# Performance work log

Hardware: AMD Instinct MI355X
Metric: run time of the kernel (lower is better)

Reference implementation:

```python
import jax, jax.numpy as jnp
from jax import lax
import numpy as np

ATTN = 32  # attn_size window
PAD, SOS = 1, 2


def setup_inputs() -> dict:
    key = jax.random.key(0)
    ks = jax.random.split(key, 20)
    B, L, V, E, H = 16, 64, 32000, 512, 512
    sc = 0.02
    inp = {
        "s_tensor": jax.random.randint(ks[0], (B, L), 0, V, dtype=jnp.int32),
        "parents_tensor": jax.random.randint(ks[1], (L,), 0, L, dtype=jnp.int32),
        "emb": jax.random.normal(ks[2], (V, E), jnp.float32) * sc,
        "W_hid": jax.random.normal(ks[3], (H, H), jnp.float32) * sc,
        "b_hid": jnp.zeros((H,), jnp.float32),
        "v_w": jax.random.normal(ks[4], (H,), jnp.float32) * sc,
        "v_b": jnp.zeros((1,), jnp.float32),
        "W_ctx": jax.random.normal(ks[5], (E + H, H), jnp.float32) * sc,
        "b_ctx": jnp.zeros((H,), jnp.float32),
        "W_ih": jax.random.normal(ks[6], (H, 4 * H), jnp.float32) * sc,
        "W_hh": jax.random.normal(ks[7], (H, 4 * H), jnp.float32) * sc,
        "b_lstm": jnp.zeros((4 * H,), jnp.float32),
        "W_glob": jax.random.normal(ks[8], (3 * H, V), jnp.float32) * sc,
        "b_glob": jnp.zeros((V,), jnp.float32),
        "w_sw": jax.random.normal(ks[9], (2 * H,), jnp.float32) * sc,
        "b_sw": jnp.zeros((1,), jnp.float32),
    }
    return inp


def _decode(emb, W_hid, b_hid, v_w, v_b, W_ctx, b_ctx, W_ih, W_hh, b_lstm,
            W_glob, b_glob, w_sw, b_sw, s_tensor, parents_tensor):
    B, L = s_tensor.shape
    H = W_hid.shape[0]
    A = ATTN
    # teacher forcing: input at step t is SOS for t=0, else s_tensor[:, t-1]
    inputs = jnp.concatenate(
        [jnp.full((B, 1), SOS, s_tensor.dtype), s_tensor[:, : L - 2]], axis=1)  # [B, L-1]
    targets = s_tensor[:, 1:]  # [B, L-1]
    hs_buf0 = jnp.zeros((B, A + L, H), jnp.float32)  # past decoder hidden states (A zero-pad prefix)
    h0 = jnp.zeros((B, H), jnp.float32)
    c0 = jnp.zeros((B, H), jnp.float32)

    def step(carry, xs):
        h, c, hs_buf = carry
        tok, tgt, par, t = xs
        x = emb[tok]  # [B, E]
        # memory = last A decoder hidden states (steps t-A .. t-1)
        mem = lax.dynamic_slice(hs_buf, (0, t, 0), (B, A, H))
        # Bahdanau-style scores: v^T tanh(W_hidden(h) + mem), masked to valid window
        q = h @ W_hid + b_hid  # [B, H]
        scores = jnp.tanh(q[:, None, :] + mem) @ v_w + v_b  # [B, A]
        valid = jnp.arange(A) >= (A - t)
        scores = jnp.where(valid[None, :], scores, -1e20)
        attn = jax.nn.softmax(scores, axis=1)
        context = jnp.einsum('ba,bah->bh', attn, mem)
        hid = jax.nn.selu(jnp.concatenate([x, context], axis=1) @ W_ctx + b_ctx)
        # single-step LSTM cell (PyTorch gate order i,f,g,o)
        gates = hid @ W_ih + h @ W_hh + b_lstm
        i, f, g, o = jnp.split(gates, 4, axis=1)
        c_new = jax.nn.sigmoid(f) * c + jax.nn.sigmoid(i) * jnp.tanh(g)
        h_new = jax.nn.sigmoid(o) * jnp.tanh(c_new)
        # parent hidden state
        p = jnp.clip(par, 0, jnp.maximum(t - 1, 0))
        h_par = lax.dynamic_slice(hs_buf, (0, A + p, 0), (B, 1, H))[:, 0]
        logits = jnp.concatenate([h_new, c_new, h_par], axis=1) @ W_glob + b_glob
        logp = jax.nn.log_softmax(logits, axis=1)
        s = jax.nn.sigmoid(jnp.concatenate([h_new, c_new], axis=1) @ w_sw + b_sw)  # [B,1]
        out = s[:, None] * logp if s.ndim == 1 else s * logp  # pointer switch on global dist
        nll = -jnp.take_along_axis(out, tgt[:, None].astype(jnp.int32), axis=1)[:, 0]
        nll = jnp.where(tgt != PAD, nll, 0.0)
        pred = jnp.argmax(out, axis=1).astype(jnp.int32)
        hs_buf = lax.dynamic_update_slice(hs_buf, h_new[:, None, :], (0, A + t, 0))
        return (h_new, c_new, hs_buf), (nll, pred)

    T = L - 1
    xs = (inputs.T, targets.T, parents_tensor[:T], jnp.arange(T, dtype=jnp.int32))
    _, (nlls, preds) = lax.scan(step, (h0, c0, hs_buf0), xs)
    loss = nlls.sum() / B
    return loss, preds.T  # [B, L-1] predicted tokens


def reference(s_tensor, parents_tensor, emb, W_hid, b_hid, v_w, v_b, W_ctx, b_ctx,
              W_ih, W_hh, b_lstm, W_glob, b_glob, w_sw, b_sw):
    return _decode(emb, W_hid, b_hid, v_w, v_b, W_ctx, b_ctx, W_ih, W_hh, b_lstm,
                   W_glob, b_glob, w_sw, b_sw, s_tensor, parents_tensor)
```

## Files before the change

kernel.cpp:

```cpp
#include <hip/hip_runtime.h>
#include <math.h>

#define BB 16
#define LL 64
#define TT 63
#define HH 512
#define AA 32
#define VV 32000
#define NCHUNK 250
#define CHW 128
#define TGRP 3
#define PAD_TOK 1
#define SOS_TOK 2
#define HSROW 96
#define ZK 1536
#define FLTMAX 3.402823466e38f

__device__ __forceinline__ float sigm(float x){ return 1.0f/(1.0f + __expf(-x)); }

__global__ __launch_bounds__(256) void k_pre(const int* __restrict__ s, const float* __restrict__ emb,
                      const float* __restrict__ Wctx, const float* __restrict__ bctx,
                      float* __restrict__ xwpre)
{
    int t = blockIdx.x >> 3;
    int jc = blockIdx.x & 7;
    int tid = threadIdx.x;
    int jj = tid & 63, bq = tid >> 6;
    int j = jc*64 + jj;
    __shared__ int toks[BB];
    __shared__ float xs[BB][HH];
    if (tid < BB) {
        int b = tid;
        toks[b] = (t == 0) ? SOS_TOK : s[b*LL + (t-1)];
    }
    __syncthreads();
    for (int i = tid; i < BB*HH; i += 256) {
        int b = i >> 9, k = i & 511;
        xs[b][k] = emb[(size_t)toks[b]*HH + k];
    }
    __syncthreads();
    float acc[4];
    #pragma unroll
    for (int u = 0; u < 4; u++) acc[u] = bctx[j];
    for (int k = 0; k < HH; k += 4) {
        float w0 = Wctx[(k+0)*HH+j], w1 = Wctx[(k+1)*HH+j],
              w2 = Wctx[(k+2)*HH+j], w3 = Wctx[(k+3)*HH+j];
        #pragma unroll
        for (int u = 0; u < 4; u++) {
            int b = bq*4 + u;
            float4 hv = *reinterpret_cast<const float4*>(&xs[b][k]);
            acc[u] = fmaf(hv.x, w0, acc[u]);
            acc[u] = fmaf(hv.y, w1, acc[u]);
            acc[u] = fmaf(hv.z, w2, acc[u]);
            acc[u] = fmaf(hv.w, w3, acc[u]);
        }
    }
    #pragma unroll
    for (int u = 0; u < 4; u++) {
        int b = bq*4 + u;
        xwpre[((size_t)t*BB + b)*HH + j] = acc[u];
    }
}

__global__ __launch_bounds__(256) void k_tw(const float* __restrict__ Wg, float4* __restrict__ Wt4b)
{
    int kg = blockIdx.x / 125;
    int cb = blockIdx.x % 125;
    int col = cb*256 + threadIdx.x;
    const float* w0 = Wg + (size_t)(4*kg)*VV + col;
    float4 v;
    v.x = w0[0];
    v.y = w0[VV];
    v.z = w0[2*VV];
    v.w = w0[3*VV];
    Wt4b[(size_t)(col >> 6)*(384*64) + kg*64 + (col & 63)] = v;
}

__global__ __launch_bounds__(256) void k_twl(const float* __restrict__ W, float4* __restrict__ WT)
{
    int kg = blockIdx.x >> 3;
    int cb = blockIdx.x & 7;
    int col = cb*256 + threadIdx.x;
    const float* w0 = W + (size_t)(4*kg)*2048 + col;
    float4 v;
    v.x = w0[0];
    v.y = w0[2048];
    v.z = w0[2*2048];
    v.w = w0[3*2048];
    WT[(size_t)kg*2048 + col] = v;
}

__device__ void finish_step(int tp, int b, int tid,
                            const int* __restrict__ s,
                            const float* __restrict__ lb,
                            const float* __restrict__ pmax,
                            const float* __restrict__ spart,
                            const float* __restrict__ bsw,
                            float* __restrict__ nll, float* __restrict__ out,
                            float* cv, int* ci, double* sdd, float* extra)
{
    float v = -FLTMAX;
    if (tid < NCHUNK) v = pmax[tid*BB + b];
    cv[tid] = v; __syncthreads();
    for (int sft = 256; sft >= 1; sft >>= 1) {
        if (tid < sft) cv[tid] = fmaxf(cv[tid], cv[tid+sft]);
        __syncthreads();
    }
    float gmax = cv[0];
    __syncthreads();

    const float* Lb = lb + (size_t)b*VV;
    double sd = 0.0;
    for (int col = tid; col < VV; col += 512) {
        float d1 = Lb[col] - gmax;
        double u = (double)d1, e;
        if (u < -0.25) {
            e = exp(u);
        } else {
            e = 1.0 + u*(1.0/7.0);
            e = 1.0 + u*e*(1.0/6.0);
            e = 1.0 + u*e*(1.0/5.0);
            e = 1.0 + u*e*(1.0/4.0);
            e = 1.0 + u*e*(1.0/3.0);
            e = 1.0 + u*e*(1.0/2.0);
            e = 1.0 + u*e;
        }
        sd += e;
    }
    sdd[tid] = sd; __syncthreads();
    for (int sft = 256; sft >= 1; sft >>= 1) {
        if (tid < sft) sdd[tid] += sdd[tid+sft];
        __syncthreads();
    }
    float logS = logf((float)sdd[0]);

    float z = bsw[0];
    #pragma unroll
    for (int i2 = 0; i2 < 8; i2++) z += spart[b*8 + i2];
    float sF = 1.0f/(1.0f + expf(-z));
    __syncthreads();

    int tg = s[b*LL + tp + 1];
    float best = -FLTMAX; int bidx = 0x7fffffff;
    for (int col = tid; col < VV; col += 512) {
        float d1 = Lb[col] - gmax;
        float d2 = d1 - logS;
        float pq = sF * d2;
        if (pq > best) { best = pq; bidx = col; }
        if (col == tg) extra[0] = pq;
    }
    cv[tid] = best; ci[tid] = bidx; __syncthreads();
    for (int sft = 256; sft >= 1; sft >>= 1) {
        if (tid < sft) {
            float v2 = cv[tid+sft]; int i2 = ci[tid+sft];
            if (v2 > cv[tid] || (v2 == cv[tid] && i2 < ci[tid])) { cv[tid] = v2; ci[tid] = i2; }
        }
        __syncthreads();
    }
    if (tid == 0) {
        out[1 + b*TT + tp] = (float)ci[0];
        nll[tp*BB + b] = (tg != PAD_TOK) ? -extra[0] : 0.f;
    }
    __syncthreads();
}

__global__ __launch_bounds__(512) void k_fin_all(
    int t0, const int* __restrict__ s,
    const float* __restrict__ lbBase, unsigned long long lbStride,
    const float* __restrict__ pmaxBase, unsigned long long pmaxStride,
    const float* __restrict__ spartAll, const float* __restrict__ bsw,
    float* __restrict__ nll, float* __restrict__ out)
{
    __shared__ float cv[512];
    __shared__ int   ci[512];
    __shared__ double sdd[512];
    __shared__ float extra[2];
    int idx = blockIdx.x >> 4;
    int tp = t0 + idx, b = blockIdx.x & 15;
    finish_step(tp, b, threadIdx.x, s,
                lbBase + (size_t)idx * lbStride,
                pmaxBase + (size_t)idx * pmaxStride,
                spartAll + (size_t)tp * 128,
                bsw, nll, out, cv, ci, sdd, extra);
}

__global__ __launch_bounds__(512) void k_attn(
    int t,
    const float* __restrict__ Whid, const float* __restrict__ bhid,
    const float* __restrict__ vw, const float* __restrict__ vb,
    const float* __restrict__ Wctx, const float* __restrict__ xwpre,
    const float* __restrict__ hs, float* __restrict__ hidg)
{
    int b = blockIdx.x, tid = threadIdx.x;
    __shared__ float hsh[HH], qs[HH], ctxs[HH];
    __shared__ float sc[AA], at[AA];
    const float* hp = hs + ((size_t)b*HSROW + (AA + t - 1))*HH;
    hsh[tid] = hp[tid];
    __syncthreads();
    {
        int j = tid;
        float acc = bhid[j];
        for (int k = 0; k < HH; k += 4) {
            float4 hv = *reinterpret_cast<const float4*>(&hsh[k]);
            acc = fmaf(hv.x, Whid[(k+0)*HH+j], acc);
            acc = fmaf(hv.y, Whid[(k+1)*HH+j], acc);
            acc = fmaf(hv.z, Whid[(k+2)*HH+j], acc);
            acc = fmaf(hv.w, Whid[(k+3)*HH+j], acc);
        }
        qs[j] = acc;
    }
    __syncthreads();
    {
        int w = tid >> 6, lane = tid & 63;
        for (int r = 0; r < 4; r++) {
            int a = w + 8*r;
            const float* mem = hs + ((size_t)b*HSROW + (t + a))*HH;
            float p = 0.f;
            for (int j = lane; j < HH; j += 64) p += tanhf(qs[j] + mem[j]) * vw[j];
            for (int m = 32; m >= 1; m >>= 1) p += __shfl_xor(p, m);
            if (lane == 0) sc[a] = (a >= AA - t) ? (p + vb[0]) : -1e20f;
        }
    }
    __syncthreads();
    if (tid < 64) {
        float v = (tid < 32) ? sc[tid] : -FLTMAX;
        float m = v;
        for (int sh = 16; sh >= 1; sh >>= 1) m = fmaxf(m, __shfl_xor(m, sh));
        float e = (tid < 32) ? __expf(v - m) : 0.f;
        float ss = e;
        for (int sh = 16; sh >= 1; sh >>= 1) ss += __shfl_xor(ss, sh);
        if (tid < 32) at[tid] = e / ss;
    }
    __syncthreads();
    {
        int j = tid;
        float ctx = 0.f;
        for (int a = 0; a < AA; a++)
            ctx += at[a] * hs[((size_t)b*HSROW + (t + a))*HH + j];
        ctxs[j] = ctx;
    }
    __syncthreads();
    {
        int j = tid;
        float acc = xwpre[((size_t)t*BB + b)*HH + j];
        const float* W2 = Wctx + (size_t)HH*HH;
        for (int k = 0; k < HH; k += 4) {
            float4 hv = *reinterpret_cast<const float4*>(&ctxs[k]);
            acc = fmaf(hv.x, W2[(k+0)*HH+j], acc);
            acc = fmaf(hv.y, W2[(k+1)*HH+j], acc);
            acc = fmaf(hv.z, W2[(k+2)*HH+j], acc);
            acc = fmaf(hv.w, W2[(k+3)*HH+j], acc);
        }
        const float scl = 1.0507009873554805f, al = 1.6732632423543772f;
        hidg[b*HH + j] = (acc > 0.f) ? scl*acc : scl*al*expm1f(acc);
    }
}

__global__ __launch_bounds__(256) void k_gates(
    int t, const int* __restrict__ parents,
    const float4* __restrict__ WihT, const float4* __restrict__ WhhT,
    const float* __restrict__ blstm, const float* __restrict__ wsw,
    const float* __restrict__ hidg, float* __restrict__ hs,
    float* __restrict__ cvec, float* __restrict__ spart,
    float* __restrict__ zbuf)
{
    int bid = blockIdx.x, b = bid >> 3, hc = bid & 7, h0 = hc*64;
    int tid = threadIdx.x, g = tid >> 6, jj = tid & 63, j = h0 + jj, col = g*HH + j;
    __shared__ float hid_s[HH], h_s[HH];
    __shared__ float gsl[4][64];
    const float* hp = hs + ((size_t)b*HSROW + (AA + t - 1))*HH;
    for (int k = tid; k < HH; k += 256) { hid_s[k] = hidg[b*HH + k]; h_s[k] = hp[k]; }
    __syncthreads();
    float acc = blstm[col];
    #pragma unroll 8
    for (int kg = 0; kg < 128; kg++) {
        float4 w = WihT[(size_t)kg*2048 + col];
        float4 hv = *reinterpret_cast<const float4*>(&hid_s[kg*4]);
        acc = fmaf(hv.x, w.x, acc);
        acc = fmaf(hv.y, w.y, acc);
        acc = fmaf(hv.z, w.z, acc);
        acc = fmaf(hv.w, w.w, acc);
    }
    #pragma unroll 8
    for (int kg = 0; kg < 128; kg++) {
        float4 w = WhhT[(size_t)kg*2048 + col];
        float4 hv = *reinterpret_cast<const float4*>(&h_s[kg*4]);
        acc = fmaf(hv.x, w.x, acc);
        acc = fmaf(hv.y, w.y, acc);
        acc = fmaf(hv.z, w.z, acc);
        acc = fmaf(hv.w, w.w, acc);
    }
    gsl[g][jj] = acc;
    __syncthreads();
    if (tid >= 64 && tid < 128) {
        int jj2 = tid - 64;
        int par = parents[t];
        int tm1 = (t - 1 > 0) ? (t - 1) : 0;
        int p = (par < 0) ? 0 : ((par > tm1) ? tm1 : par);
        float v = (t == 0) ? 0.f : hs[((size_t)b*HSROW + (AA + p))*HH + h0 + jj2];
        zbuf[(size_t)b*ZK + 2*HH + h0 + jj2] = v;
    }
    if (tid < 64) {
        float gi = gsl[0][jj], gf = gsl[1][jj], gg = gsl[2][jj], go = gsl[3][jj];
        float cp = cvec[b*HH + j];
        float cn = sigm(gf)*cp + sigm(gi)*tanhf(gg);
        float hn = sigm(go)*tanhf(cn);
        cvec[b*HH + j] = cn;
        hs[((size_t)b*HSROW + (AA + t))*HH + j] = hn;
        zbuf[(size_t)b*ZK + j] = hn;
        zbuf[(size_t)b*ZK + HH + j] = cn;
        float sp = hn*wsw[j] + cn*wsw[HH + j];
        for (int m = 32; m >= 1; m >>= 1) sp += __shfl_xor(sp, m);
        if (jj == 0) spart[b*8 + hc] = sp;
    }
}

template<int NT>
__device__ __forceinline__ void logits_body2(
    const float4* __restrict__ Wt4b, const float* __restrict__ bg,
    const float* __restrict__ zBase, size_t zStride,
    float* __restrict__ lbBase, size_t lbStride,
    float* __restrict__ pmaxBase, size_t pmaxStride)
{
    int tid = threadIdx.x;
    int chunk = blockIdx.y;
    int lane = tid & 63;
    int cg = lane & 31;
    int kh = lane >> 5;
    int b0 = (tid >> 6) * 4;
    int base_t = blockIdx.x * NT;

    const float4* wt0 = Wt4b + (size_t)(chunk*2 + 0)*(384*64) + cg;
    const float4* wt1 = Wt4b + (size_t)(chunk*2 + 0)*(384*64) + cg + 32;
    const float4* wt2 = Wt4b + (size_t)(chunk*2 + 1)*(384*64) + cg;
    const float4* wt3 = Wt4b + (size_t)(chunk*2 + 1)*(384*64) + cg + 32;

    float acc[NT][4][4];
    #pragma unroll
    for (int tt = 0; tt < NT; tt++)
        #pragma unroll
        for (int cc = 0; cc < 4; cc++) {
            float binit = (kh == 0) ? bg[chunk*CHW + cg + 32*cc] : 0.f;
            #pragma unroll
            for (int u = 0; u < 4; u++) acc[tt][cc][u] = binit;
        }

    for (int kc = 0; kc < 3; kc++) {
        const float* zb[NT];
        #pragma unroll
        for (int tt = 0; tt < NT; tt++)
            zb[tt] = zBase + (size_t)(base_t + tt)*zStride + kc*512 + (size_t)b0*ZK;
        int kgb = kc*128 + kh*64;
        #pragma unroll 2
        for (int k4 = 0; k4 < 64; k4++) {
            int kb = kh*256 + k4*4;
            size_t wof = (size_t)(kgb + k4)*64;
            float4 w0 = wt0[wof];
            float4 w1 = wt1[wof];
            float4 w2 = wt2[wof];
            float4 w3 = wt3[wof];
            #pragma unroll
            for (int tt = 0; tt < NT; tt++) {
                #pragma unroll
                for (int u = 0; u < 4; u++) {
                    float4 z = *reinterpret_cast<const float4*>(&zb[tt][(size_t)u*ZK + kb]);
                    acc[tt][0][u] = fmaf(z.x, w0.x, fmaf(z.y, w0.y, fmaf(z.z, w0.z, fmaf(z.w, w0.w, acc[tt][0][u]))));
                    acc[tt][1][u] = fmaf(z.x, w1.x, fmaf(z.y, w1.y, fmaf(z.z, w1.z, fmaf(z.w, w1.w, acc[tt][1][u]))));
                    acc[tt][2][u] = fmaf(z.x, w2.x, fmaf(z.y, w2.y, fmaf(z.z, w2.z, fmaf(z.w, w2.w, acc[tt][2][u]))));
                    acc[tt][3][u] = fmaf(z.x, w3.x, fmaf(z.y, w3.y, fmaf(z.z, w3.z, fmaf(z.w, w3.w, acc[tt][3][u]))));
                }
            }
        }
    }

    #pragma unroll
    for (int tt = 0; tt < NT; tt++) {
        float* lb   = lbBase   + (size_t)(base_t + tt)*lbStride;
        float* pmax = pmaxBase + (size_t)(base_t + tt)*pmaxStride;
        #pragma unroll
        for (int u = 0; u < 4; u++) {
            float vmax = -FLTMAX;
            #pragma unroll
            for (int cc = 0; cc < 4; cc++) {
                float a = acc[tt][cc][u];
                float oth = __shfl_xor(a, 32);
                float tot = a + oth;
                if (kh == 0) lb[(size_t)(b0 + u)*VV + chunk*CHW + cg + 32*cc] = tot;
                vmax = fmaxf(vmax, tot);
            }
            for (int m = 16; m >= 1; m >>= 1) vmax = fmaxf(vmax, __shfl_xor(vmax, m));
            if (lane == 0) pmax[chunk*BB + b0 + u] = vmax;
        }
    }
}

__global__ __launch_bounds__(256) void k_logits_mega3(
    const float4* __restrict__ Wt4b, const float* __restrict__ bg,
    const float* __restrict__ zBase,
    float* __restrict__ lbBase, float* __restrict__ pmaxBase)
{
    logits_body2<TGRP>(Wt4b, bg, zBase, (size_t)BB*ZK, lbBase, 512000, pmaxBase, 4000);
}

__global__ __launch_bounds__(256) void k_logits_T1(
    const float4* __restrict__ Wt4b, const float* __restrict__ bg,
    const float* __restrict__ zbuf,
    float* __restrict__ lb, float* __restrict__ pmax)
{
    logits_body2<1>(Wt4b, bg, zbuf, 0, lb, 0, pmax, 0);
}

__global__ __launch_bounds__(256) void k_logits_F(
    const float* __restrict__ Wg, const float* __restrict__ bg,
    const float* __restrict__ zbuf,
    float* __restrict__ lb, float* __restrict__ pmax)
{
    int tid = threadIdx.x;
    int chunk = blockIdx.y;
    int lane = tid & 63;
    int cg = lane & 31;
    int kh = lane >> 5;
    int b0 = (tid >> 6) * 4;

    float acc[4][4];
    #pragma unroll
    for (int cc = 0; cc < 4; cc++) {
        float binit = (kh == 0) ? bg[chunk*CHW + cg + 32*cc] : 0.f;
        #pragma unroll
        for (int u = 0; u < 4; u++) acc[cc][u] = binit;
    }

    for (int kc = 0; kc < 3; kc++) {
        const float* zb = zbuf + kc*512 + (size_t)b0*ZK;
        #pragma unroll 2
        for (int k4 = 0; k4 < 64; k4++) {
            int kb = kh*256 + k4*4;
            const float* wr = Wg + (size_t)(kc*512 + kb)*VV + chunk*CHW + cg;
            float4 w[4];
            #pragma unroll
            for (int cc = 0; cc < 4; cc++) {
                w[cc].x = wr[32*cc];
                w[cc].y = wr[(size_t)VV + 32*cc];
                w[cc].z = wr[(size_t)2*VV + 32*cc];
                w[cc].w = wr[(size_t)3*VV + 32*cc];
            }
            #pragma unroll
            for (int u = 0; u < 4; u++) {
                float4 z = *reinterpret_cast<const float4*>(&zb[(size_t)u*ZK + kb]);
                #pragma unroll
                for (int cc = 0; cc < 4; cc++)
                    acc[cc][u] = fmaf(z.x, w[cc].x, fmaf(z.y, w[cc].y, fmaf(z.z, w[cc].z, fmaf(z.w, w[cc].w, acc[cc][u]))));
            }
        }
    }

    #pragma unroll
    for (int u = 0; u < 4; u++) {
        float vmax = -FLTMAX;
        #pragma unroll
        for (int cc = 0; cc < 4; cc++) {
            float a = acc[cc][u];
            float oth = __shfl_xor(a, 32);
            float tot = a + oth;
            if (kh == 0) lb[(size_t)(b0 + u)*VV + chunk*CHW + cg + 32*cc] = tot;
            vmax = fmaxf(vmax, tot);
        }
        for (int m = 16; m >= 1; m >>= 1) vmax = fmaxf(vmax, __shfl_xor(vmax, m));
        if (lane == 0) pmax[chunk*BB + b0 + u] = vmax;
    }
}

__global__ __launch_bounds__(256) void k_final_loss(
    const float* __restrict__ nll, float* __restrict__ out)
{
    __shared__ double cs2[256];
    int tid = threadIdx.x;
    double psm = 0.0;
    for (int i = tid; i < TT*BB; i += 256) psm += (double)nll[i];
    cs2[tid] = psm; __syncthreads();
    for (int sft = 128; sft >= 1; sft >>= 1) {
        if (tid < sft) cs2[tid] += cs2[tid+sft];
        __syncthreads();
    }
    if (tid == 0) out[0] = (float)(cs2[0] / (double)BB);
}

extern "C" void kernel_launch(void* const* d_in, const int* in_sizes, int n_in,
                              void* d_out, int out_size, void* d_ws, size_t ws_size,
                              hipStream_t stream)
{
    const int*   s_tok = (const int*)  d_in[0];
    const int*   par   = (const int*)  d_in[1];
    const float* emb   = (const float*)d_in[2];
    const float* Whid  = (const float*)d_in[3];
    const float* bhid  = (const float*)d_in[4];
    const float* vw    = (const float*)d_in[5];
    const float* vb    = (const float*)d_in[6];
    const float* Wctx  = (const float*)d_in[7];
    const float* bctx  = (const float*)d_in[8];
    const float* Wih   = (const float*)d_in[9];
    const float* Whh   = (const float*)d_in[10];
    const float* blstm = (const float*)d_in[11];
    const float* Wg    = (const float*)d_in[12];
    const float* bg    = (const float*)d_in[13];
    const float* wsw   = (const float*)d_in[14];
    const float* bsw   = (const float*)d_in[15];
    float* out = (float*)d_out;

    size_t ws_f = ws_size / sizeof(float);
    const size_t base_f = 786432 + 8192 + 516096 + 8192;
    const size_t com_f  = 8064 + 1008 + 2*1048576;
    const size_t full_f = base_f + com_f + (size_t)63*4000 + (size_t)63*512000
                        + (size_t)63*24576 + 49152000;
    const size_t mid_f  = base_f + com_f + 4000 + 512000 + 24576 + 49152000;
    int mode = (ws_f >= full_f) ? 2 : ((ws_f >= mid_f) ? 1 : 0);

    float* ws = (float*)d_ws;
    size_t off = 0;
    float* hs      = ws + off; off += 786432;
    float* cvec    = ws + off; off += 8192;
    float* xwpre   = ws + off; off += 516096;
    float* hidg    = ws + off; off += 8192;
    float* pmaxAll = ws + off; off += (mode == 2) ? (size_t)63*4000 : 4000;
    float* spartAll= ws + off; off += 8064;
    float* nll     = ws + off; off += 1008;
    float* zbufAll = ws + off; off += (mode == 2) ? (size_t)63*24576 : 24576;
    float* lbAll   = ws + off; off += (mode == 2) ? (size_t)63*512000 : 512000;
    float4* WihT   = (float4*)(ws + off); off += 1048576;
    float4* WhhT   = (float4*)(ws + off); off += 1048576;
    float4* Wt4b   = (float4*)(ws + off);

    hipMemsetAsync(hs, 0, (786432 + 8192) * sizeof(float), stream);

    hipLaunchKernelGGL(k_twl, dim3(1024), dim3(256), 0, stream, Wih, WihT);
    hipLaunchKernelGGL(k_twl, dim3(1024), dim3(256), 0, stream, Whh, WhhT);
    if (mode >= 1) {
        hipLaunchKernelGGL(k_tw, dim3(384*125), dim3(256), 0, stream, Wg, Wt4b);
    }
    hipLaunchKernelGGL(k_pre, dim3(TT*8), dim3(256), 0, stream, s_tok, emb, Wctx, bctx, xwpre);

    if (mode == 2) {
        for (int t = 0; t < TT; t++) {
            hipLaunchKernelGGL(k_attn, dim3(BB), dim3(512), 0, stream,
                t, Whid, bhid, vw, vb, Wctx, xwpre, hs, hidg);
            hipLaunchKernelGGL(k_gates, dim3(128), dim3(256), 0, stream,
                t, par, WihT, WhhT, blstm, wsw, hidg, hs, cvec,
                spartAll + (size_t)t*128, zbufAll + (size_t)t*BB*ZK);
        }
        hipLaunchKernelGGL(k_logits_mega3, dim3(TT/TGRP, NCHUNK), dim3(256), 0, stream,
            Wt4b, bg, zbufAll, lbAll, pmaxAll);
        hipLaunchKernelGGL(k_fin_all, dim3(TT*BB), dim3(512), 0, stream,
            0, s_tok, lbAll, (unsigned long long)512000,
            pmaxAll, (unsigned long long)4000,
            spartAll, bsw, nll, out);
    } else {
        for (int t = 0; t < TT; t++) {
            hipLaunchKernelGGL(k_attn, dim3(BB), dim3(512), 0, stream,
                t, Whid, bhid, vw, vb, Wctx, xwpre, hs, hidg);
            hipLaunchKernelGGL(k_gates, dim3(128), dim3(256), 0, stream,
                t, par, WihT, WhhT, blstm, wsw, hidg, hs, cvec,
                spartAll + (size_t)t*128, zbufAll);
            if (mode >= 1) {
                hipLaunchKernelGGL(k_logits_T1, dim3(1, NCHUNK), dim3(256), 0, stream,
                    Wt4b, bg, zbufAll, lbAll, pmaxAll);
            } else {
                hipLaunchKernelGGL(k_logits_F, dim3(1, NCHUNK), dim3(256), 0, stream,
                    Wg, bg, zbufAll, lbAll, pmaxAll);
            }
            hipLaunchKernelGGL(k_fin_all, dim3(BB), dim3(512), 0, stream,
                t, s_tok, lbAll, (unsigned long long)0, pmaxAll, (unsigned long long)0,
                spartAll, bsw, nll, out);
        }
    }
    hipLaunchKernelGGL(k_final_loss, dim3(1), dim3(256), 0, stream, nll, out);
}
```

Measured before the change: 5.353 ms.

## Fuse attention and LSTM gate kernels per step, remap logits grid, nontemporal stores

Merges k_attn and k_gates into one k_step kernel launched on 128 blocks. Each block redundantly recomputes the per-batch attention and hidden projection, then computes its own 64-column slice of the gates. This halves the launches per step and drops the hidg global round trip, at the cost of 8x redundant attention work per batch. The logits mega-kernel now uses a 1D grid that interleaves chunk/time-group work across XCDs, and the logit stores become nontemporal to avoid polluting cache.

```diff
diff --git a/kernel.cpp b/kernel.cpp
--- a/kernel.cpp
+++ b/kernel.cpp
@@ -10,6 +10,7 @@
 #define NCHUNK 250
 #define CHW 128
 #define TGRP 3
+#define NTG 21
 #define PAD_TOK 1
 #define SOS_TOK 2
 #define HSROW 96
@@ -184,21 +185,31 @@
                 bsw, nll, out, cv, ci, sdd, extra);
 }
 
-__global__ __launch_bounds__(512) void k_attn(
-    int t,
+__global__ __launch_bounds__(256) void k_step(
+    int t, const int* __restrict__ parents,
     const float* __restrict__ Whid, const float* __restrict__ bhid,
     const float* __restrict__ vw, const float* __restrict__ vb,
     const float* __restrict__ Wctx, const float* __restrict__ xwpre,
-    const float* __restrict__ hs, float* __restrict__ hidg)
-{
-    int b = blockIdx.x, tid = threadIdx.x;
-    __shared__ float hsh[HH], qs[HH], ctxs[HH];
+    const float4* __restrict__ WihT, const float4* __restrict__ WhhT,
+    const float* __restrict__ blstm, const float* __restrict__ wsw,
+    float* __restrict__ hs, float* __restrict__ cvec,
+    float* __restrict__ spart, float* __restrict__ zbuf)
+{
+    int bid = blockIdx.x, b = bid >> 3, hc = bid & 7, h0 = hc*64;
+    int tid = threadIdx.x;
+    __shared__ float hsh[HH], qs[HH], ctxs[HH], hid_s[HH];
     __shared__ float sc[AA], at[AA];
+    __shared__ float gsl[4][64];
+    const float* W2 = Wctx + (size_t)HH*HH;
+
     const float* hp = hs + ((size_t)b*HSROW + (AA + t - 1))*HH;
     hsh[tid] = hp[tid];
-    __syncthreads();
-    {
-        int j = tid;
+    hsh[tid + 256] = hp[tid + 256];
+    __syncthreads();
+
+    #pragma unroll
+    for (int jo = 0; jo < HH; jo += 256) {
+        int j = tid + jo;
         float acc = bhid[j];
         for (int k = 0; k < HH; k += 4) {
             float4 hv = *reinterpret_cast<const float4*>(&hsh[k]);
@@ -210,10 +221,11 @@
         qs[j] = acc;
     }
     __syncthreads();
+
     {
         int w = tid >> 6, lane = tid & 63;
-        for (int r = 0; r < 4; r++) {
-            int a = w + 8*r;
+        for (int r = 0; r < 8; r++) {
+            int a = w + 4*r;
             const float* mem = hs + ((size_t)b*HSROW + (t + a))*HH;
             float p = 0.f;
             for (int j = lane; j < HH; j += 64) p += tanhf(qs[j] + mem[j]) * vw[j];
@@ -222,6 +234,7 @@
         }
     }
     __syncthreads();
+
     if (tid < 64) {
         float v = (tid < 32) ? sc[tid] : -FLTMAX;
         float m = v;
@@ -232,18 +245,21 @@
         if (tid < 32) at[tid] = e / ss;
     }
     __syncthreads();
-    {
-        int j = tid;
+
+    #pragma unroll
+    for (int jo = 0; jo < HH; jo += 256) {
+        int j = tid + jo;
         float ctx = 0.f;
         for (int a = 0; a < AA; a++)
             ctx += at[a] * hs[((size_t)b*HSROW + (t + a))*HH + j];
         ctxs[j] = ctx;
     }
     __syncthreads();
-    {
-        int j = tid;
+
+    #pragma unroll
+    for (int jo = 0; jo < HH; jo += 256) {
+        int j = tid + jo;
         float acc = xwpre[((size_t)t*BB + b)*HH + j];
-        const float* W2 = Wctx + (size_t)HH*HH;
         for (int k = 0; k < HH; k += 4) {
             float4 hv = *reinterpret_cast<const float4*>(&ctxs[k]);
             acc = fmaf(hv.x, W2[(k+0)*HH+j], acc);
@@ -252,45 +268,33 @@
             acc = fmaf(hv.w, W2[(k+3)*HH+j], acc);
         }
         const float scl = 1.0507009873554805f, al = 1.6732632423543772f;
-        hidg[b*HH + j] = (acc > 0.f) ? scl*acc : scl*al*expm1f(acc);
-    }
-}
-
-__global__ __launch_bounds__(256) void k_gates(
-    int t, const int* __restrict__ parents,
-    const float4* __restrict__ WihT, const float4* __restrict__ WhhT,
-    const float* __restrict__ blstm, const float* __restrict__ wsw,
-    const float* __restrict__ hidg, float* __restrict__ hs,
-    float* __restrict__ cvec, float* __restrict__ spart,
-    float* __restrict__ zbuf)
-{
-    int bid = blockIdx.x, b = bid >> 3, hc = bid & 7, h0 = hc*64;
-    int tid = threadIdx.x, g = tid >> 6, jj = tid & 63, j = h0 + jj, col = g*HH + j;
-    __shared__ float hid_s[HH], h_s[HH];
-    __shared__ float gsl[4][64];
-    const float* hp = hs + ((size_t)b*HSROW + (AA + t - 1))*HH;
-    for (int k = tid; k < HH; k += 256) { hid_s[k] = hidg[b*HH + k]; h_s[k] = hp[k]; }
-    __syncthreads();
-    float acc = blstm[col];
-    #pragma unroll 8
-    for (int kg = 0; kg < 128; kg++) {
-        float4 w = WihT[(size_t)kg*2048 + col];
-        float4 hv = *reinterpret_cast<const float4*>(&hid_s[kg*4]);
-        acc = fmaf(hv.x, w.x, acc);
-        acc = fmaf(hv.y, w.y, acc);
-        acc = fmaf(hv.z, w.z, acc);
-        acc = fmaf(hv.w, w.w, acc);
-    }
-    #pragma unroll 8
-    for (int kg = 0; kg < 128; kg++) {
-        float4 w = WhhT[(size_t)kg*2048 + col];
-        float4 hv = *reinterpret_cast<const float4*>(&h_s[kg*4]);
-        acc = fmaf(hv.x, w.x, acc);
-        acc = fmaf(hv.y, w.y, acc);
-        acc = fmaf(hv.z, w.z, acc);
-        acc = fmaf(hv.w, w.w, acc);
-    }
-    gsl[g][jj] = acc;
+        hid_s[j] = (acc > 0.f) ? scl*acc : scl*al*expm1f(acc);
+    }
+    __syncthreads();
+
+    {
+        int g = tid >> 6, jj = tid & 63, j = h0 + jj, col = g*HH + j;
+        float acc = blstm[col];
+        #pragma unroll 8
+        for (int kg = 0; kg < 128; kg++) {
+            float4 w = WihT[(size_t)kg*2048 + col];
+            float4 hv = *reinterpret_cast<const float4*>(&hid_s[kg*4]);
+            acc = fmaf(hv.x, w.x, acc);
+            acc = fmaf(hv.y, w.y, acc);
+            acc = fmaf(hv.z, w.z, acc);
+            acc = fmaf(hv.w, w.w, acc);
+        }
+        #pragma unroll 8
+        for (int kg = 0; kg < 128; kg++) {
+            float4 w = WhhT[(size_t)kg*2048 + col];
+            float4 hv = *reinterpret_cast<const float4*>(&hsh[kg*4]);
+            acc = fmaf(hv.x, w.x, acc);
+            acc = fmaf(hv.y, w.y, acc);
+            acc = fmaf(hv.z, w.z, acc);
+            acc = fmaf(hv.w, w.w, acc);
+        }
+        gsl[g][jj] = acc;
+    }
     __syncthreads();
     if (tid >= 64 && tid < 128) {
         int jj2 = tid - 64;
@@ -301,6 +305,7 @@
         zbuf[(size_t)b*ZK + 2*HH + h0 + jj2] = v;
     }
     if (tid < 64) {
+        int jj = tid & 63, j = h0 + jj;
         float gi = gsl[0][jj], gf = gsl[1][jj], gg = gsl[2][jj], go = gsl[3][jj];
         float cp = cvec[b*HH + j];
         float cn = sigm(gf)*cp + sigm(gi)*tanhf(gg);
@@ -316,19 +321,17 @@
 }
 
 template<int NT>
-__device__ __forceinline__ void logits_body2(
+__device__ __forceinline__ void logits_body2(int chunk, int base_t,
     const float4* __restrict__ Wt4b, const float* __restrict__ bg,
     const float* __restrict__ zBase, size_t zStride,
     float* __restrict__ lbBase, size_t lbStride,
     float* __restrict__ pmaxBase, size_t pmaxStride)
 {
     int tid = threadIdx.x;
-    int chunk = blockIdx.y;
     int lane = tid & 63;
     int cg = lane & 31;
     int kh = lane >> 5;
     int b0 = (tid >> 6) * 4;
-    int base_t = blockIdx.x * NT;
 
     const float4* wt0 = Wt4b + (size_t)(chunk*2 + 0)*(384*64) + cg;
     const float4* wt1 = Wt4b + (size_t)(chunk*2 + 0)*(384*64) + cg + 32;
@@ -385,7 +388,8 @@
                 float a = acc[tt][cc][u];
                 float oth = __shfl_xor(a, 32);
                 float tot = a + oth;
-                if (kh == 0) lb[(size_t)(b0 + u)*VV + chunk*CHW + cg + 32*cc] = tot;
+                if (kh == 0)
+                    __builtin_nontemporal_store(tot, &lb[(size_t)(b0 + u)*VV + chunk*CHW + cg + 32*cc]);
                 vmax = fmaxf(vmax, tot);
             }
             for (int m = 16; m >= 1; m >>= 1) vmax = fmaxf(vmax, __shfl_xor(vmax, m));
@@ -399,7 +403,14 @@
     const float* __restrict__ zBase,
     float* __restrict__ lbBase, float* __restrict__ pmaxBase)
 {
-    logits_body2<TGRP>(Wt4b, bg, zBase, (size_t)BB*ZK, lbBase, 512000, pmaxBase, 4000);
+    int h = blockIdx.x;
+    int r = h & 7, m = h >> 3;
+    int w = r*672 + m;
+    if (w >= NTG*NCHUNK) return;
+    int chunk = w / NTG;
+    int base_t = (w % NTG) * TGRP;
+    logits_body2<TGRP>(chunk, base_t, Wt4b, bg, zBase, (size_t)BB*ZK,
+                       lbBase, 512000, pmaxBase, 4000);
 }
 
 __global__ __launch_bounds__(256) void k_logits_T1(
@@ -407,7 +418,7 @@
     const float* __restrict__ zbuf,
     float* __restrict__ lb, float* __restrict__ pmax)
 {
-    logits_body2<1>(Wt4b, bg, zbuf, 0, lb, 0, pmax, 0);
+    logits_body2<1>(blockIdx.x, 0, Wt4b, bg, zbuf, 0, lb, 0, pmax, 0);
 }
 
 __global__ __launch_bounds__(256) void k_logits_F(
@@ -416,7 +427,7 @@
     float* __restrict__ lb, float* __restrict__ pmax)
 {
     int tid = threadIdx.x;
-    int chunk = blockIdx.y;
+    int chunk = blockIdx.x;
     int lane = tid & 63;
     int cg = lane & 31;
     int kh = lane >> 5;
@@ -508,7 +519,7 @@
     float* out = (float*)d_out;
 
     size_t ws_f = ws_size / sizeof(float);
-    const size_t base_f = 786432 + 8192 + 516096 + 8192;
+    const size_t base_f = 786432 + 8192 + 516096;
     const size_t com_f  = 8064 + 1008 + 2*1048576;
     const size_t full_f = base_f + com_f + (size_t)63*4000 + (size_t)63*512000
                         + (size_t)63*24576 + 49152000;
@@ -520,7 +531,6 @@
     float* hs      = ws + off; off += 786432;
     float* cvec    = ws + off; off += 8192;
     float* xwpre   = ws + off; off += 516096;
-    float* hidg    = ws + off; off += 8192;
     float* pmaxAll = ws + off; off += (mode == 2) ? (size_t)63*4000 : 4000;
     float* spartAll= ws + off; off += 8064;
     float* nll     = ws + off; off += 1008;
@@ -541,13 +551,11 @@
 
     if (mode == 2) {
         for (int t = 0; t < TT; t++) {
-            hipLaunchKernelGGL(k_attn, dim3(BB), dim3(512), 0, stream,
-                t, Whid, bhid, vw, vb, Wctx, xwpre, hs, hidg);
-            hipLaunchKernelGGL(k_gates, dim3(128), dim3(256), 0, stream,
-                t, par, WihT, WhhT, blstm, wsw, hidg, hs, cvec,
-                spartAll + (size_t)t*128, zbufAll + (size_t)t*BB*ZK);
-        }
-        hipLaunchKernelGGL(k_logits_mega3, dim3(TT/TGRP, NCHUNK), dim3(256), 0, stream,
+            hipLaunchKernelGGL(k_step, dim3(128), dim3(256), 0, stream,
+                t, par, Whid, bhid, vw, vb, Wctx, xwpre, WihT, WhhT, blstm, wsw,
+                hs, cvec, spartAll + (size_t)t*128, zbufAll + (size_t)t*BB*ZK);
+        }
+        hipLaunchKernelGGL(k_logits_mega3, dim3(8*672), dim3(256), 0, stream,
             Wt4b, bg, zbufAll, lbAll, pmaxAll);
         hipLaunchKernelGGL(k_fin_all, dim3(TT*BB), dim3(512), 0, stream,
             0, s_tok, lbAll, (unsigned long long)512000,
@@ -555,16 +563,14 @@
             spartAll, bsw, nll, out);
     } else {
         for (int t = 0; t < TT; t++) {
-            hipLaunchKernelGGL(k_attn, dim3(BB), dim3(512), 0, stream,
-                t, Whid, bhid, vw, vb, Wctx, xwpre, hs, hidg);
-            hipLaunchKernelGGL(k_gates, dim3(128), dim3(256), 0, stream,
-                t, par, WihT, WhhT, blstm, wsw, hidg, hs, cvec,
-                spartAll + (size_t)t*128, zbufAll);
+            hipLaunchKernelGGL(k_step, dim3(128), dim3(256), 0, stream,
+                t, par, Whid, bhid, vw, vb, Wctx, xwpre, WihT, WhhT, blstm, wsw,
+                hs, cvec, spartAll + (size_t)t*128, zbufAll);
             if (mode >= 1) {
-                hipLaunchKernelGGL(k_logits_T1, dim3(1, NCHUNK), dim3(256), 0, stream,
+                hipLaunchKernelGGL(k_logits_T1, dim3(NCHUNK), dim3(256), 0, stream,
                     Wt4b, bg, zbufAll, lbAll, pmaxAll);
             } else {
-                hipLaunchKernelGGL(k_logits_F, dim3(1, NCHUNK), dim3(256), 0, stream,
+                hipLaunchKernelGGL(k_logits_F, dim3(NCHUNK), dim3(256), 0, stream,
                     Wg, bg, zbufAll, lbAll, pmaxAll);
             }
             hipLaunchKernelGGL(k_fin_all, dim3(BB), dim3(512), 0, stream,
```

Result: slower. 8.297 ms (+55.0%).

## Restructure logits GEMM: per-wave K split with LDS reduction, XCD-aware block mapping

Applied to the files above, without the earlier changes.

Reworks the logits kernels so each wave owns a K-half and 8 batch rows across 128 contiguous columns. This replaces lane-level K splitting with a cross-wave reduction through shared memory, and each lane loads two float4 weights instead of four. The mega kernel also gets a 1D grid whose block indices are remapped so neighbouring chunks land on the same XCD, and logits are written with nontemporal stores. It adds __syncthreads barriers and LDS traffic, and raises per-thread accumulator count, which could hurt occupancy.

```diff
diff --git a/kernel.cpp b/kernel.cpp
--- a/kernel.cpp
+++ b/kernel.cpp
@@ -10,6 +10,7 @@
 #define NCHUNK 250
 #define CHW 128
 #define TGRP 3
+#define NTG 21
 #define PAD_TOK 1
 #define SOS_TOK 2
 #define HSROW 96
@@ -316,58 +317,54 @@
 }
 
 template<int NT>
-__device__ __forceinline__ void logits_body2(
+__device__ __forceinline__ void logits_body3(int chunk, int base_t,
     const float4* __restrict__ Wt4b, const float* __restrict__ bg,
     const float* __restrict__ zBase, size_t zStride,
     float* __restrict__ lbBase, size_t lbStride,
-    float* __restrict__ pmaxBase, size_t pmaxStride)
+    float* __restrict__ pmaxBase, size_t pmaxStride,
+    float* red)
 {
     int tid = threadIdx.x;
-    int chunk = blockIdx.y;
     int lane = tid & 63;
-    int cg = lane & 31;
-    int kh = lane >> 5;
-    int b0 = (tid >> 6) * 4;
-    int base_t = blockIdx.x * NT;
-
-    const float4* wt0 = Wt4b + (size_t)(chunk*2 + 0)*(384*64) + cg;
-    const float4* wt1 = Wt4b + (size_t)(chunk*2 + 0)*(384*64) + cg + 32;
-    const float4* wt2 = Wt4b + (size_t)(chunk*2 + 1)*(384*64) + cg;
-    const float4* wt3 = Wt4b + (size_t)(chunk*2 + 1)*(384*64) + cg + 32;
-
-    float acc[NT][4][4];
-    #pragma unroll
-    for (int tt = 0; tt < NT; tt++)
-        #pragma unroll
-        for (int cc = 0; cc < 4; cc++) {
-            float binit = (kh == 0) ? bg[chunk*CHW + cg + 32*cc] : 0.f;
+    int wave = __builtin_amdgcn_readfirstlane(tid >> 6);
+    int kh = wave & 1;
+    int b0 = (wave >> 1) * 8;
+
+    const float4* wtA = Wt4b + (size_t)(chunk*2 + 0)*(384*64) + lane;
+    const float4* wtB = Wt4b + (size_t)(chunk*2 + 1)*(384*64) + lane;
+
+    float acc[NT][2][8];
+    {
+        float bi0 = (kh == 0) ? bg[chunk*CHW + lane] : 0.f;
+        float bi1 = (kh == 0) ? bg[chunk*CHW + 64 + lane] : 0.f;
+        #pragma unroll
+        for (int tt = 0; tt < NT; tt++)
             #pragma unroll
-            for (int u = 0; u < 4; u++) acc[tt][cc][u] = binit;
-        }
+            for (int u = 0; u < 8; u++) { acc[tt][0][u] = bi0; acc[tt][1][u] = bi1; }
+    }
 
     for (int kc = 0; kc < 3; kc++) {
-        const float* zb[NT];
+        const float* zq[NT][8];
         #pragma unroll
         for (int tt = 0; tt < NT; tt++)
-            zb[tt] = zBase + (size_t)(base_t + tt)*zStride + kc*512 + (size_t)b0*ZK;
+            #pragma unroll
+            for (int u = 0; u < 8; u++)
+                zq[tt][u] = zBase + (size_t)(base_t + tt)*zStride + kc*512
+                          + (size_t)(b0 + u)*ZK + kh*256;
         int kgb = kc*128 + kh*64;
-        #pragma unroll 2
+        const float4* waP = wtA + (size_t)kgb*64;
+        const float4* wbP = wtB + (size_t)kgb*64;
+        #pragma unroll 4
         for (int k4 = 0; k4 < 64; k4++) {
-            int kb = kh*256 + k4*4;
-            size_t wof = (size_t)(kgb + k4)*64;
-            float4 w0 = wt0[wof];
-            float4 w1 = wt1[wof];
-            float4 w2 = wt2[wof];
-            float4 w3 = wt3[wof];
+            float4 wa = waP[k4*64];
+            float4 wb = wbP[k4*64];
             #pragma unroll
             for (int tt = 0; tt < NT; tt++) {
                 #pragma unroll
-                for (int u = 0; u < 4; u++) {
-                    float4 z = *reinterpret_cast<const float4*>(&zb[tt][(size_t)u*ZK + kb]);
-                    acc[tt][0][u] = fmaf(z.x, w0.x, fmaf(z.y, w0.y, fmaf(z.z, w0.z, fmaf(z.w, w0.w, acc[tt][0][u]))));
-                    acc[tt][1][u] = fmaf(z.x, w1.x, fmaf(z.y, w1.y, fmaf(z.z, w1.z, fmaf(z.w, w1.w, acc[tt][1][u]))));
-                    acc[tt][2][u] = fmaf(z.x, w2.x, fmaf(z.y, w2.y, fmaf(z.z, w2.z, fmaf(z.w, w2.w, acc[tt][2][u]))));
-                    acc[tt][3][u] = fmaf(z.x, w3.x, fmaf(z.y, w3.y, fmaf(z.z, w3.z, fmaf(z.w, w3.w, acc[tt][3][u]))));
+                for (int u = 0; u < 8; u++) {
+                    float4 z = *reinterpret_cast<const float4*>(zq[tt][u] + k4*4);
+                    acc[tt][0][u] = fmaf(z.x, wa.x, fmaf(z.y, wa.y, fmaf(z.z, wa.z, fmaf(z.w, wa.w, acc[tt][0][u]))));
+                    acc[tt][1][u] = fmaf(z.x, wb.x, fmaf(z.y, wb.y, fmaf(z.z, wb.z, fmaf(z.w, wb.w, acc[tt][1][u]))));
                 }
             }
         }
@@ -375,22 +372,29 @@
 
     #pragma unroll
     for (int tt = 0; tt < NT; tt++) {
-        float* lb   = lbBase   + (size_t)(base_t + tt)*lbStride;
-        float* pmax = pmaxBase + (size_t)(base_t + tt)*pmaxStride;
-        #pragma unroll
-        for (int u = 0; u < 4; u++) {
-            float vmax = -FLTMAX;
+        if (kh == 1) {
             #pragma unroll
-            for (int cc = 0; cc < 4; cc++) {
-                float a = acc[tt][cc][u];
-                float oth = __shfl_xor(a, 32);
-                float tot = a + oth;
-                if (kh == 0) lb[(size_t)(b0 + u)*VV + chunk*CHW + cg + 32*cc] = tot;
-                vmax = fmaxf(vmax, tot);
+            for (int u = 0; u < 8; u++) {
+                red[(b0 + u)*128 + lane]      = acc[tt][0][u];
+                red[(b0 + u)*128 + 64 + lane] = acc[tt][1][u];
             }
-            for (int m = 16; m >= 1; m >>= 1) vmax = fmaxf(vmax, __shfl_xor(vmax, m));
-            if (lane == 0) pmax[chunk*BB + b0 + u] = vmax;
-        }
+        }
+        __syncthreads();
+        if (kh == 0) {
+            float* lb   = lbBase   + (size_t)(base_t + tt)*lbStride;
+            float* pmax = pmaxBase + (size_t)(base_t + tt)*pmaxStride;
+            #pragma unroll
+            for (int u = 0; u < 8; u++) {
+                float t0 = acc[tt][0][u] + red[(b0 + u)*128 + lane];
+                float t1 = acc[tt][1][u] + red[(b0 + u)*128 + 64 + lane];
+                __builtin_nontemporal_store(t0, &lb[(size_t)(b0 + u)*VV + chunk*CHW + lane]);
+                __builtin_nontemporal_store(t1, &lb[(size_t)(b0 + u)*VV + chunk*CHW + 64 + lane]);
+                float vmax = fmaxf(t0, t1);
+                for (int m = 32; m >= 1; m >>= 1) vmax = fmaxf(vmax, __shfl_xor(vmax, m));
+                if (lane == 0) pmax[chunk*BB + b0 + u] = vmax;
+            }
+        }
+        __syncthreads();
     }
 }
 
@@ -399,7 +403,15 @@
     const float* __restrict__ zBase,
     float* __restrict__ lbBase, float* __restrict__ pmaxBase)
 {
-    logits_body2<TGRP>(Wt4b, bg, zBase, (size_t)BB*ZK, lbBase, 512000, pmaxBase, 4000);
+    __shared__ float red[BB*128];
+    int h = blockIdx.x;
+    int r = h & 7, m = h >> 3;
+    int w = r*672 + m;
+    if (w >= NTG*NCHUNK) return;
+    int chunk = w / NTG;
+    int base_t = (w % NTG) * TGRP;
+    logits_body3<TGRP>(chunk, base_t, Wt4b, bg, zBase, (size_t)BB*ZK,
+                       lbBase, 512000, pmaxBase, 4000, red);
 }
 
 __global__ __launch_bounds__(256) void k_logits_T1(
@@ -407,7 +419,8 @@
     const float* __restrict__ zbuf,
     float* __restrict__ lb, float* __restrict__ pmax)
 {
-    logits_body2<1>(Wt4b, bg, zbuf, 0, lb, 0, pmax, 0);
+    __shared__ float red[BB*128];
+    logits_body3<1>(blockIdx.x, 0, Wt4b, bg, zbuf, 0, lb, 0, pmax, 0, red);
 }
 
 __global__ __launch_bounds__(256) void k_logits_F(
@@ -415,58 +428,65 @@
     const float* __restrict__ zbuf,
     float* __restrict__ lb, float* __restrict__ pmax)
 {
+    __shared__ float red[BB*128];
     int tid = threadIdx.x;
-    int chunk = blockIdx.y;
+    int chunk = blockIdx.x;
     int lane = tid & 63;
-    int cg = lane & 31;
-    int kh = lane >> 5;
-    int b0 = (tid >> 6) * 4;
-
-    float acc[4][4];
-    #pragma unroll
-    for (int cc = 0; cc < 4; cc++) {
-        float binit = (kh == 0) ? bg[chunk*CHW + cg + 32*cc] : 0.f;
-        #pragma unroll
-        for (int u = 0; u < 4; u++) acc[cc][u] = binit;
+    int wave = __builtin_amdgcn_readfirstlane(tid >> 6);
+    int kh = wave & 1;
+    int b0 = (wave >> 1) * 8;
+    int col0 = chunk*CHW + lane, col1 = col0 + 64;
+
+    float acc[2][8];
+    {
+        float bi0 = (kh == 0) ? bg[col0] : 0.f;
+        float bi1 = (kh == 0) ? bg[col1] : 0.f;
+        #pragma unroll
+        for (int u = 0; u < 8; u++) { acc[0][u] = bi0; acc[1][u] = bi1; }
     }
 
     for (int kc = 0; kc < 3; kc++) {
-        const float* zb = zbuf + kc*512 + (size_t)b0*ZK;
+        const float* zq[8];
+        #pragma unroll
+        for (int u = 0; u < 8; u++)
+            zq[u] = zbuf + kc*512 + (size_t)(b0 + u)*ZK + kh*256;
         #pragma unroll 2
         for (int k4 = 0; k4 < 64; k4++) {
             int kb = kh*256 + k4*4;
-            const float* wr = Wg + (size_t)(kc*512 + kb)*VV + chunk*CHW + cg;
-            float4 w[4];
+            const float* wr = Wg + (size_t)(kc*512 + kb)*VV;
+            float4 wa, wb;
+            wa.x = wr[col0]; wa.y = wr[(size_t)VV + col0];
+            wa.z = wr[(size_t)2*VV + col0]; wa.w = wr[(size_t)3*VV + col0];
+            wb.x = wr[col1]; wb.y = wr[(size_t)VV + col1];
+            wb.z = wr[(size_t)2*VV + col1]; wb.w = wr[(size_t)3*VV + col1];
             #pragma unroll
-            for (int cc = 0; cc < 4; cc++) {
-                w[cc].x = wr[32*cc];
-                w[cc].y = wr[(size_t)VV + 32*cc];
-                w[cc].z = wr[(size_t)2*VV + 32*cc];
-                w[cc].w = wr[(size_t)3*VV + 32*cc];
+            for (int u = 0; u < 8; u++) {
+                float4 z = *reinterpret_cast<const float4*>(zq[u] + k4*4);
+                acc[0][u] = fmaf(z.x, wa.x, fmaf(z.y, wa.y, fmaf(z.z, wa.z, fmaf(z.w, wa.w, acc[0][u]))));
+                acc[1][u] = fmaf(z.x, wb.x, fmaf(z.y, wb.y, fmaf(z.z, wb.z, fmaf(z.w, wb.w, acc[1][u]))));
             }
-            #pragma unroll
-            for (int u = 0; u < 4; u++) {
-                float4 z = *reinterpret_cast<const float4*>(&zb[(size_t)u*ZK + kb]);
-                #pragma unroll
-                for (int cc = 0; cc < 4; cc++)
-                    acc[cc][u] = fmaf(z.x, w[cc].x, fmaf(z.y, w[cc].y, fmaf(z.z, w[cc].z, fmaf(z.w, w[cc].w, acc[cc][u]))));
-            }
-        }
-    }
-
-    #pragma unroll
-    for (int u = 0; u < 4; u++) {
-        float vmax = -FLTMAX;
-        #pragma unroll
-        for (int cc = 0; cc < 4; cc++) {
-            float a = acc[cc][u];
-            float oth = __shfl_xor(a, 32);
-            float tot = a + oth;
-            if (kh == 0) lb[(size_t)(b0 + u)*VV + chunk*CHW + cg + 32*cc] = tot;
-            vmax = fmaxf(vmax, tot);
-        }
-        for (int m = 16; m >= 1; m >>= 1) vmax = fmaxf(vmax, __shfl_xor(vmax, m));
-        if (lane == 0) pmax[chunk*BB + b0 + u] = vmax;
+        }
+    }
+
+    if (kh == 1) {
+        #pragma unroll
+        for (int u = 0; u < 8; u++) {
+            red[(b0 + u)*128 + lane]      = acc[0][u];
+            red[(b0 + u)*128 + 64 + lane] = acc[1][u];
+        }
+    }
+    __syncthreads();
+    if (kh == 0) {
+        #pragma unroll
+        for (int u = 0; u < 8; u++) {
+            float t0 = acc[0][u] + red[(b0 + u)*128 + lane];
+            float t1 = acc[1][u] + red[(b0 + u)*128 + 64 + lane];
+            lb[(size_t)(b0 + u)*VV + col0] = t0;
+            lb[(size_t)(b0 + u)*VV + col1] = t1;
+            float vmax = fmaxf(t0, t1);
+            for (int m = 32; m >= 1; m >>= 1) vmax = fmaxf(vmax, __shfl_xor(vmax, m));
+            if (lane == 0) pmax[chunk*BB + b0 + u] = vmax;
+        }
     }
 }
 
@@ -547,7 +567,7 @@
                 t, par, WihT, WhhT, blstm, wsw, hidg, hs, cvec,
                 spartAll + (size_t)t*128, zbufAll + (size_t)t*BB*ZK);
         }
-        hipLaunchKernelGGL(k_logits_mega3, dim3(TT/TGRP, NCHUNK), dim3(256), 0, stream,
+        hipLaunchKernelGGL(k_logits_mega3, dim3(8*672), dim3(256), 0, stream,
             Wt4b, bg, zbufAll, lbAll, pmaxAll);
         hipLaunchKernelGGL(k_fin_all, dim3(TT*BB), dim3(512), 0, stream,
             0, s_tok, lbAll, (unsigned long long)512000,
@@ -561,10 +581,10 @@
                 t, par, WihT, WhhT, blstm, wsw, hidg, hs, cvec,
                 spartAll + (size_t)t*128, zbufAll);
             if (mode >= 1) {
-                hipLaunchKernelGGL(k_logits_T1, dim3(1, NCHUNK), dim3(256), 0, stream,
+                hipLaunchKernelGGL(k_logits_T1, dim3(NCHUNK), dim3(256), 0, stream,
                     Wt4b, bg, zbufAll, lbAll, pmaxAll);
             } else {
-                hipLaunchKernelGGL(k_logits_F, dim3(1, NCHUNK), dim3(256), 0, stream,
+                hipLaunchKernelGGL(k_logits_F, dim3(NCHUNK), dim3(256), 0, stream,
                     Wg, bg, zbufAll, lbAll, pmaxAll);
             }
             hipLaunchKernelGGL(k_fin_all, dim3(BB), dim3(512), 0, stream,
```

Result: slower. 5.604 ms (+4.7%).
